# Kernel optimization log

Hardware: AMD Instinct MI355X
Metric: run time of the kernel (lower is better)

The kernel has to match this reference:

```python
import jax, jax.numpy as jnp
import numpy as np

N = 100000  # nodes
E = 800000  # edges (before self-loops)
D = 64      # in_dim == out_dim


def setup_inputs() -> dict:
    key = jax.random.key(0)
    k_x, k_e, k_w, k_b = jax.random.split(key, 4)
    x = jax.random.normal(k_x, (N, D), dtype=jnp.float32)
    edge_index = jax.random.randint(k_e, (2, E), 0, N, dtype=jnp.int64)
    # GCNConv linear params (PyG: glorot weight, zero bias; random here)
    W = jax.random.normal(k_w, (D, D), dtype=jnp.float32) / np.sqrt(D)
    b = jax.random.normal(k_b, (D,), dtype=jnp.float32) * 0.01
    return {"x": x, "W": W, "b": b, "edge_index": edge_index}


def reference(x, W, b, edge_index):
    n = x.shape[0]
    # GCNConv: linear transform first
    h = x @ W.T  # [N, D]
    # add self-loops (PyG default add_self_loops=True)
    loops = jnp.arange(n, dtype=edge_index.dtype)
    src = jnp.concatenate([edge_index[0], loops])
    dst = jnp.concatenate([edge_index[1], loops])
    # symmetric normalization D^{-1/2} A D^{-1/2} (degrees include self-loops)
    deg = jax.ops.segment_sum(jnp.ones_like(dst, dtype=h.dtype), dst, num_segments=n)
    dinv = jnp.where(deg > 0, jax.lax.rsqrt(deg), 0.0)
    norm = dinv[src] * dinv[dst]  # [E+N]
    # gather -> scale -> scatter-add
    msg = h[src] * norm[:, None]  # [E+N, D]
    agg = jax.ops.segment_sum(msg, dst, num_segments=n) + b  # [N, D]
    # residual (in_dim == out_dim -> identity residual) + ReLU
    return jax.nn.relu(agg + x)
```

## Files before the change

### kernel.cpp

```cpp
#include <hip/hip_runtime.h>


#define NN 100000
#define NE 800000
#define DD 64
#define CAP 32
#define CHUNK 1024
#define NCHUNK ((NE + CHUNK - 1) / CHUNK)

typedef unsigned int uint;
typedef unsigned short ushort;

__device__ __forceinline__ ushort f2bf(float f) {
    uint u = __float_as_uint(f);
    u += 0x7fffu + ((u >> 16) & 1u);
    return (ushort)(u >> 16);
}
__device__ __forceinline__ float bflo(uint u) { return __uint_as_float(u << 16); }
__device__ __forceinline__ float bfhi(uint u) { return __uint_as_float(u & 0xffff0000u); }

__global__ __launch_bounds__(256) void fill_kernel(const int* __restrict__ ei,
                                                   int* __restrict__ cur,
                                                   int* __restrict__ srcIdx) {
    int g = blockIdx.x & 7;
    int chunk = blockIdx.x >> 3;
    int base = chunk * CHUNK + threadIdx.x * 4;
    if (base >= NE) return;
    int4 dv = *(const int4*)(ei + NE + base);
    int dd[4] = {dv.x, dv.y, dv.z, dv.w};
#pragma unroll
    for (int j = 0; j < 4; ++j) {
        int d = dd[j];
        if ((d & 7) == g) {
            int s = ei[base + j];
            int c = atomicAdd(&cur[d], 1);
            if (c < CAP) srcIdx[(d << 5) + c] = s;
        }
    }
}

__global__ __launch_bounds__(256) void linear_kernel(const float4* __restrict__ x4g,
                                                     const float* __restrict__ W,
                                                     const int* __restrict__ deg,
                                                     ushort4* __restrict__ hq4) {
    __shared__ float4 wt4[64 * 16];
    __shared__ float4 xs4[64 * 17];
    int t = threadIdx.x;

    float* wt = (float*)wt4;
    for (int m = t; m < 4096; m += 256)
        wt[m] = W[(m & 63) * 64 + (m >> 6)];

    int rowBase = blockIdx.x * 64;
    for (int m = t; m < 1024; m += 256) {
        int rl = m >> 4;
        xs4[rl * 17 + (m & 15)] = (rowBase + rl < NN)
            ? x4g[(size_t)rowBase * 16 + m]
            : make_float4(0.f, 0.f, 0.f, 0.f);
    }
    __syncthreads();

    int tc = t & 15;
    int tr = t >> 4;
    float4 acc[4];
#pragma unroll
    for (int i = 0; i < 4; ++i) acc[i] = make_float4(0.f, 0.f, 0.f, 0.f);

#pragma unroll 2
    for (int kq = 0; kq < 16; ++kq) {
        float4 w0 = wt4[(kq * 4 + 0) * 16 + tc];
        float4 w1 = wt4[(kq * 4 + 1) * 16 + tc];
        float4 w2 = wt4[(kq * 4 + 2) * 16 + tc];
        float4 w3 = wt4[(kq * 4 + 3) * 16 + tc];
#pragma unroll
        for (int i = 0; i < 4; ++i) {
            float4 xv = xs4[(tr * 4 + i) * 17 + kq];
            acc[i].x += xv.x * w0.x + xv.y * w1.x + xv.z * w2.x + xv.w * w3.x;
            acc[i].y += xv.x * w0.y + xv.y * w1.y + xv.z * w2.y + xv.w * w3.y;
            acc[i].z += xv.x * w0.z + xv.y * w1.z + xv.z * w2.z + xv.w * w3.z;
            acc[i].w += xv.x * w0.w + xv.y * w1.w + xv.z * w2.w + xv.w * w3.w;
        }
    }

#pragma unroll
    for (int i = 0; i < 4; ++i) {
        int g = rowBase + tr * 4 + i;
        if (g < NN) {
            float sc = rsqrtf((float)deg[g] + 1.0f);
            ushort4 o;
            o.x = f2bf(acc[i].x * sc); o.y = f2bf(acc[i].y * sc);
            o.z = f2bf(acc[i].z * sc); o.w = f2bf(acc[i].w * sc);
            hq4[(size_t)g * 16 + tc] = o;
        }
    }
}

__global__ __launch_bounds__(256) void gather_kernel(const int* __restrict__ srcIdx,
                                                     const int* __restrict__ deg,
                                                     const uint4* __restrict__ hq4,
                                                     const float4* __restrict__ x4,
                                                     const float* __restrict__ b,
                                                     float4* __restrict__ out4) {
    int t = blockIdx.x * blockDim.x + threadIdx.x;
    int node = t >> 3;
    int l = t & 7;
    if (node >= NN) return;

    int dg = deg[node];
    float di = rsqrtf((float)dg + 1.0f);
    if (dg > CAP) dg = CAP;
    int beg = node << 5;
    int end = beg + dg;

    float acc[8];
    uint4 v = hq4[(size_t)node * 8 + l];
    acc[0] = bflo(v.x); acc[1] = bfhi(v.x);
    acc[2] = bflo(v.y); acc[3] = bfhi(v.y);
    acc[4] = bflo(v.z); acc[5] = bfhi(v.z);
    acc[6] = bflo(v.w); acc[7] = bfhi(v.w);

    int p = beg;
    for (; p + 4 <= end; p += 4) {
        int s0 = srcIdx[p];
        int s1 = srcIdx[p + 1];
        int s2 = srcIdx[p + 2];
        int s3 = srcIdx[p + 3];
        uint4 v0 = hq4[(size_t)s0 * 8 + l];
        uint4 v1 = hq4[(size_t)s1 * 8 + l];
        uint4 v2 = hq4[(size_t)s2 * 8 + l];
        uint4 v3 = hq4[(size_t)s3 * 8 + l];
        acc[0] += bflo(v0.x); acc[1] += bfhi(v0.x);
        acc[2] += bflo(v0.y); acc[3] += bfhi(v0.y);
        acc[4] += bflo(v0.z); acc[5] += bfhi(v0.z);
        acc[6] += bflo(v0.w); acc[7] += bfhi(v0.w);
        acc[0] += bflo(v1.x); acc[1] += bfhi(v1.x);
        acc[2] += bflo(v1.y); acc[3] += bfhi(v1.y);
        acc[4] += bflo(v1.z); acc[5] += bfhi(v1.z);
        acc[6] += bflo(v1.w); acc[7] += bfhi(v1.w);
        acc[0] += bflo(v2.x); acc[1] += bfhi(v2.x);
        acc[2] += bflo(v2.y); acc[3] += bfhi(v2.y);
        acc[4] += bflo(v2.z); acc[5] += bfhi(v2.z);
        acc[6] += bflo(v2.w); acc[7] += bfhi(v2.w);
        acc[0] += bflo(v3.x); acc[1] += bfhi(v3.x);
        acc[2] += bflo(v3.y); acc[3] += bfhi(v3.y);
        acc[4] += bflo(v3.z); acc[5] += bfhi(v3.z);
        acc[6] += bflo(v3.w); acc[7] += bfhi(v3.w);
    }
    for (; p < end; ++p) {
        int s0 = srcIdx[p];
        uint4 v0 = hq4[(size_t)s0 * 8 + l];
        acc[0] += bflo(v0.x); acc[1] += bfhi(v0.x);
        acc[2] += bflo(v0.y); acc[3] += bfhi(v0.y);
        acc[4] += bflo(v0.z); acc[5] += bfhi(v0.z);
        acc[6] += bflo(v0.w); acc[7] += bfhi(v0.w);
    }

    float4 xa = x4[(size_t)node * 16 + l * 2];
    float4 xb = x4[(size_t)node * 16 + l * 2 + 1];
    float4 oa, ob;
    int cb = l * 8;
    oa.x = fmaxf(di * acc[0] + b[cb + 0] + xa.x, 0.f);
    oa.y = fmaxf(di * acc[1] + b[cb + 1] + xa.y, 0.f);
    oa.z = fmaxf(di * acc[2] + b[cb + 2] + xa.z, 0.f);
    oa.w = fmaxf(di * acc[3] + b[cb + 3] + xa.w, 0.f);
    ob.x = fmaxf(di * acc[4] + b[cb + 4] + xb.x, 0.f);
    ob.y = fmaxf(di * acc[5] + b[cb + 5] + xb.y, 0.f);
    ob.z = fmaxf(di * acc[6] + b[cb + 6] + xb.z, 0.f);
    ob.w = fmaxf(di * acc[7] + b[cb + 7] + xb.w, 0.f);
    out4[(size_t)node * 16 + l * 2]     = oa;
    out4[(size_t)node * 16 + l * 2 + 1] = ob;
}

extern "C" void kernel_launch(void* const* d_in, const int* in_sizes, int n_in,
                              void* d_out, int out_size, void* d_ws, size_t ws_size,
                              hipStream_t stream) {
    const float* x = (const float*)d_in[0];
    const float* W = (const float*)d_in[1];
    const float* b = (const float*)d_in[2];
    const int* ei = (const int*)d_in[3];

    char* ws = (char*)d_ws;
    int*    cur    = (int*)(ws + 0);
    int*    srcIdx = (int*)(ws + 400000);
    ushort* hq     = (ushort*)(ws + 13200000);

    hipMemsetAsync(cur, 0, NN * sizeof(int), stream);

    fill_kernel<<<NCHUNK * 8, 256, 0, stream>>>(ei, cur, srcIdx);
    linear_kernel<<<(NN + 63) / 64, 256, 0, stream>>>((const float4*)x, W, cur,
                                                      (ushort4*)hq);
    gather_kernel<<<NN / 32, 256, 0, stream>>>(srcIdx, cur, (const uint4*)hq,
                                               (const float4*)x, b, (float4*)d_out);
}
```

Before: 167.0 us.

## Fuse zero, fill, linear and dinv phases into one cooperative persistent kernel

Replaces the memset, fill kernel and linear kernel with a single cooperative-launch persistent kernel that zeroes degree counters, builds the bucketed adjacency, runs the linear transform and computes dinv, separated by grid-wide syncs. The linear output is no longer pre-scaled by the source degree, so it no longer has to wait for the degree counts. This lets the linear transform overlap with the atomic fill. The gather kernel now loads a per-source dinv value and multiplies it into every accumulated message, adding one extra random load and more multiplies per edge. The goal is to remove launch overhead and inter-kernel serialization, at the cost of grid syncs and a heavier inner gather loop.

```diff
diff --git a/kernel.cpp b/kernel.cpp
--- a/kernel.cpp
+++ b/kernel.cpp
@@ -1,12 +1,16 @@
 #include <hip/hip_runtime.h>
+#include <hip/hip_cooperative_groups.h>
+
+namespace cg = cooperative_groups;
 
 
 #define NN 100000
 #define NE 800000
-#define DD 64
 #define CAP 32
 #define CHUNK 1024
 #define NCHUNK ((NE + CHUNK - 1) / CHUNK)
+#define NUNIT (NCHUNK * 8)
+#define NTILE ((NN + 63) / 64)
 
 typedef unsigned int uint;
 typedef unsigned short ushort;
@@ -19,30 +23,38 @@
 __device__ __forceinline__ float bflo(uint u) { return __uint_as_float(u << 16); }
 __device__ __forceinline__ float bfhi(uint u) { return __uint_as_float(u & 0xffff0000u); }
 
-__global__ __launch_bounds__(256) void fill_kernel(const int* __restrict__ ei,
-                                                   int* __restrict__ cur,
-                                                   int* __restrict__ srcIdx) {
-    int g = blockIdx.x & 7;
-    int chunk = blockIdx.x >> 3;
-    int base = chunk * CHUNK + threadIdx.x * 4;
-    if (base >= NE) return;
-    int4 dv = *(const int4*)(ei + NE + base);
-    int dd[4] = {dv.x, dv.y, dv.z, dv.w};
-#pragma unroll
-    for (int j = 0; j < 4; ++j) {
-        int d = dd[j];
-        if ((d & 7) == g) {
-            int s = ei[base + j];
-            int c = atomicAdd(&cur[d], 1);
-            if (c < CAP) srcIdx[(d << 5) + c] = s;
-        }
-    }
-}
-
-__global__ __launch_bounds__(256) void linear_kernel(const float4* __restrict__ x4g,
-                                                     const float* __restrict__ W,
-                                                     const int* __restrict__ deg,
-                                                     ushort4* __restrict__ hq4) {
+
+__device__ __forceinline__ void zero_phase(int* __restrict__ cur, int bid, int grid) {
+    for (int i = bid * 256 + (int)threadIdx.x; i < NN; i += grid * 256) cur[i] = 0;
+}
+
+__device__ __forceinline__ void fill_phase(const int* __restrict__ ei,
+                                           int* __restrict__ cur,
+                                           int* __restrict__ srcIdx,
+                                           int bid, int grid) {
+    int g = bid & 7;
+    for (int u = bid; u < NUNIT; u += grid) {
+        int base = (u >> 3) * CHUNK + (int)threadIdx.x * 4;
+        if (base < NE) {
+            int4 dv = *(const int4*)(ei + NE + base);
+            int dd[4] = {dv.x, dv.y, dv.z, dv.w};
+#pragma unroll
+            for (int j = 0; j < 4; ++j) {
+                int d = dd[j];
+                if ((d & 7) == g) {
+                    int s = ei[base + j];
+                    int c = atomicAdd(&cur[d], 1);
+                    if (c < CAP) srcIdx[(d << 5) + c] = s;
+                }
+            }
+        }
+    }
+}
+
+__device__ __forceinline__ void linear_phase(const float4* __restrict__ x4g,
+                                             const float* __restrict__ W,
+                                             ushort4* __restrict__ hq4,
+                                             int bid, int grid) {
     __shared__ float4 wt4[64 * 16];
     __shared__ float4 xs4[64 * 17];
     int t = threadIdx.x;
@@ -51,52 +63,93 @@
     for (int m = t; m < 4096; m += 256)
         wt[m] = W[(m & 63) * 64 + (m >> 6)];
 
-    int rowBase = blockIdx.x * 64;
-    for (int m = t; m < 1024; m += 256) {
-        int rl = m >> 4;
-        xs4[rl * 17 + (m & 15)] = (rowBase + rl < NN)
-            ? x4g[(size_t)rowBase * 16 + m]
-            : make_float4(0.f, 0.f, 0.f, 0.f);
-    }
-    __syncthreads();
-
-    int tc = t & 15;
-    int tr = t >> 4;
-    float4 acc[4];
-#pragma unroll
-    for (int i = 0; i < 4; ++i) acc[i] = make_float4(0.f, 0.f, 0.f, 0.f);
+    for (int tile = bid; tile < NTILE; tile += grid) {
+        __syncthreads();
+        int rowBase = tile * 64;
+        for (int m = t; m < 1024; m += 256) {
+            int rl = m >> 4;
+            xs4[rl * 17 + (m & 15)] = (rowBase + rl < NN)
+                ? x4g[(size_t)rowBase * 16 + m]
+                : make_float4(0.f, 0.f, 0.f, 0.f);
+        }
+        __syncthreads();
+
+        int tc = t & 15;
+        int tr = t >> 4;
+        float4 acc[4];
+#pragma unroll
+        for (int i = 0; i < 4; ++i) acc[i] = make_float4(0.f, 0.f, 0.f, 0.f);
 
 #pragma unroll 2
-    for (int kq = 0; kq < 16; ++kq) {
-        float4 w0 = wt4[(kq * 4 + 0) * 16 + tc];
-        float4 w1 = wt4[(kq * 4 + 1) * 16 + tc];
-        float4 w2 = wt4[(kq * 4 + 2) * 16 + tc];
-        float4 w3 = wt4[(kq * 4 + 3) * 16 + tc];
+        for (int kq = 0; kq < 16; ++kq) {
+            float4 w0 = wt4[(kq * 4 + 0) * 16 + tc];
+            float4 w1 = wt4[(kq * 4 + 1) * 16 + tc];
+            float4 w2 = wt4[(kq * 4 + 2) * 16 + tc];
+            float4 w3 = wt4[(kq * 4 + 3) * 16 + tc];
+#pragma unroll
+            for (int i = 0; i < 4; ++i) {
+                float4 xv = xs4[(tr * 4 + i) * 17 + kq];
+                acc[i].x += xv.x * w0.x + xv.y * w1.x + xv.z * w2.x + xv.w * w3.x;
+                acc[i].y += xv.x * w0.y + xv.y * w1.y + xv.z * w2.y + xv.w * w3.y;
+                acc[i].z += xv.x * w0.z + xv.y * w1.z + xv.z * w2.z + xv.w * w3.z;
+                acc[i].w += xv.x * w0.w + xv.y * w1.w + xv.z * w2.w + xv.w * w3.w;
+            }
+        }
+
 #pragma unroll
         for (int i = 0; i < 4; ++i) {
-            float4 xv = xs4[(tr * 4 + i) * 17 + kq];
-            acc[i].x += xv.x * w0.x + xv.y * w1.x + xv.z * w2.x + xv.w * w3.x;
-            acc[i].y += xv.x * w0.y + xv.y * w1.y + xv.z * w2.y + xv.w * w3.y;
-            acc[i].z += xv.x * w0.z + xv.y * w1.z + xv.z * w2.z + xv.w * w3.z;
-            acc[i].w += xv.x * w0.w + xv.y * w1.w + xv.z * w2.w + xv.w * w3.w;
-        }
-    }
-
-#pragma unroll
-    for (int i = 0; i < 4; ++i) {
-        int g = rowBase + tr * 4 + i;
-        if (g < NN) {
-            float sc = rsqrtf((float)deg[g] + 1.0f);
-            ushort4 o;
-            o.x = f2bf(acc[i].x * sc); o.y = f2bf(acc[i].y * sc);
-            o.z = f2bf(acc[i].z * sc); o.w = f2bf(acc[i].w * sc);
-            hq4[(size_t)g * 16 + tc] = o;
-        }
-    }
+            int gr = rowBase + tr * 4 + i;
+            if (gr < NN) {
+                ushort4 o;
+                o.x = f2bf(acc[i].x); o.y = f2bf(acc[i].y);
+                o.z = f2bf(acc[i].z); o.w = f2bf(acc[i].w);
+                hq4[(size_t)gr * 16 + tc] = o;
+            }
+        }
+    }
+}
+
+__device__ __forceinline__ void dinv_phase(const int* __restrict__ cur,
+                                           float* __restrict__ dinv,
+                                           int bid, int grid) {
+    for (int i = bid * 256 + (int)threadIdx.x; i < NN; i += grid * 256)
+        dinv[i] = rsqrtf((float)cur[i] + 1.0f);
+}
+
+__global__ __launch_bounds__(256, 4) void fused_kernel(const int* __restrict__ ei,
+                                                       const float4* __restrict__ x4g,
+                                                       const float* __restrict__ W,
+                                                       int* __restrict__ cur,
+                                                       int* __restrict__ srcIdx,
+                                                       ushort4* __restrict__ hq4,
+                                                       float* __restrict__ dinv) {
+    cg::grid_group gg = cg::this_grid();
+    int bid = blockIdx.x, grid = gridDim.x;
+    zero_phase(cur, bid, grid);
+    gg.sync();
+    fill_phase(ei, cur, srcIdx, bid, grid);
+    linear_phase(x4g, W, hq4, bid, grid);
+    gg.sync();
+    dinv_phase(cur, dinv, bid, grid);
+}
+
+__global__ __launch_bounds__(256) void zero_kernel(int* cur) {
+    zero_phase(cur, blockIdx.x, gridDim.x);
+}
+__global__ __launch_bounds__(256) void fill_kernel(const int* ei, int* cur, int* srcIdx) {
+    fill_phase(ei, cur, srcIdx, blockIdx.x, gridDim.x);
+}
+__global__ __launch_bounds__(256) void linear_kernel(const float4* x4g, const float* W,
+                                                     ushort4* hq4) {
+    linear_phase(x4g, W, hq4, blockIdx.x, gridDim.x);
+}
+__global__ __launch_bounds__(256) void dinv_kernel(const int* cur, float* dinv) {
+    dinv_phase(cur, dinv, blockIdx.x, gridDim.x);
 }
 
 __global__ __launch_bounds__(256) void gather_kernel(const int* __restrict__ srcIdx,
                                                      const int* __restrict__ deg,
+                                                     const float* __restrict__ dinv,
                                                      const uint4* __restrict__ hq4,
                                                      const float4* __restrict__ x4,
                                                      const float* __restrict__ b,
@@ -107,17 +160,17 @@
     if (node >= NN) return;
 
     int dg = deg[node];
-    float di = rsqrtf((float)dg + 1.0f);
+    float di = dinv[node];
     if (dg > CAP) dg = CAP;
     int beg = node << 5;
     int end = beg + dg;
 
     float acc[8];
     uint4 v = hq4[(size_t)node * 8 + l];
-    acc[0] = bflo(v.x); acc[1] = bfhi(v.x);
-    acc[2] = bflo(v.y); acc[3] = bfhi(v.y);
-    acc[4] = bflo(v.z); acc[5] = bfhi(v.z);
-    acc[6] = bflo(v.w); acc[7] = bfhi(v.w);
+    acc[0] = di * bflo(v.x); acc[1] = di * bfhi(v.x);
+    acc[2] = di * bflo(v.y); acc[3] = di * bfhi(v.y);
+    acc[4] = di * bflo(v.z); acc[5] = di * bfhi(v.z);
+    acc[6] = di * bflo(v.w); acc[7] = di * bfhi(v.w);
 
     int p = beg;
     for (; p + 4 <= end; p += 4) {
@@ -125,34 +178,36 @@
         int s1 = srcIdx[p + 1];
         int s2 = srcIdx[p + 2];
         int s3 = srcIdx[p + 3];
+        float w0 = dinv[s0], w1 = dinv[s1], w2 = dinv[s2], w3 = dinv[s3];
         uint4 v0 = hq4[(size_t)s0 * 8 + l];
         uint4 v1 = hq4[(size_t)s1 * 8 + l];
         uint4 v2 = hq4[(size_t)s2 * 8 + l];
         uint4 v3 = hq4[(size_t)s3 * 8 + l];
-        acc[0] += bflo(v0.x); acc[1] += bfhi(v0.x);
-        acc[2] += bflo(v0.y); acc[3] += bfhi(v0.y);
-        acc[4] += bflo(v0.z); acc[5] += bfhi(v0.z);
-        acc[6] += bflo(v0.w); acc[7] += bfhi(v0.w);
-        acc[0] += bflo(v1.x); acc[1] += bfhi(v1.x);
-        acc[2] += bflo(v1.y); acc[3] += bfhi(v1.y);
-        acc[4] += bflo(v1.z); acc[5] += bfhi(v1.z);
-        acc[6] += bflo(v1.w); acc[7] += bfhi(v1.w);
-        acc[0] += bflo(v2.x); acc[1] += bfhi(v2.x);
-        acc[2] += bflo(v2.y); acc[3] += bfhi(v2.y);
-        acc[4] += bflo(v2.z); acc[5] += bfhi(v2.z);
-        acc[6] += bflo(v2.w); acc[7] += bfhi(v2.w);
-        acc[0] += bflo(v3.x); acc[1] += bfhi(v3.x);
-        acc[2] += bflo(v3.y); acc[3] += bfhi(v3.y);
-        acc[4] += bflo(v3.z); acc[5] += bfhi(v3.z);
-        acc[6] += bflo(v3.w); acc[7] += bfhi(v3.w);
+        acc[0] += w0 * bflo(v0.x); acc[1] += w0 * bfhi(v0.x);
+        acc[2] += w0 * bflo(v0.y); acc[3] += w0 * bfhi(v0.y);
+        acc[4] += w0 * bflo(v0.z); acc[5] += w0 * bfhi(v0.z);
+        acc[6] += w0 * bflo(v0.w); acc[7] += w0 * bfhi(v0.w);
+        acc[0] += w1 * bflo(v1.x); acc[1] += w1 * bfhi(v1.x);
+        acc[2] += w1 * bflo(v1.y); acc[3] += w1 * bfhi(v1.y);
+        acc[4] += w1 * bflo(v1.z); acc[5] += w1 * bfhi(v1.z);
+        acc[6] += w1 * bflo(v1.w); acc[7] += w1 * bfhi(v1.w);
+        acc[0] += w2 * bflo(v2.x); acc[1] += w2 * bfhi(v2.x);
+        acc[2] += w2 * bflo(v2.y); acc[3] += w2 * bfhi(v2.y);
+        acc[4] += w2 * bflo(v2.z); acc[5] += w2 * bfhi(v2.z);
+        acc[6] += w2 * bflo(v2.w); acc[7] += w2 * bfhi(v2.w);
+        acc[0] += w3 * bflo(v3.x); acc[1] += w3 * bfhi(v3.x);
+        acc[2] += w3 * bflo(v3.y); acc[3] += w3 * bfhi(v3.y);
+        acc[4] += w3 * bflo(v3.z); acc[5] += w3 * bfhi(v3.z);
+        acc[6] += w3 * bflo(v3.w); acc[7] += w3 * bfhi(v3.w);
     }
     for (; p < end; ++p) {
         int s0 = srcIdx[p];
+        float w0 = dinv[s0];
         uint4 v0 = hq4[(size_t)s0 * 8 + l];
-        acc[0] += bflo(v0.x); acc[1] += bfhi(v0.x);
-        acc[2] += bflo(v0.y); acc[3] += bfhi(v0.y);
-        acc[4] += bflo(v0.z); acc[5] += bfhi(v0.z);
-        acc[6] += bflo(v0.w); acc[7] += bfhi(v0.w);
+        acc[0] += w0 * bflo(v0.x); acc[1] += w0 * bfhi(v0.x);
+        acc[2] += w0 * bflo(v0.y); acc[3] += w0 * bfhi(v0.y);
+        acc[4] += w0 * bflo(v0.z); acc[5] += w0 * bfhi(v0.z);
+        acc[6] += w0 * bflo(v0.w); acc[7] += w0 * bfhi(v0.w);
     }
 
     float4 xa = x4[(size_t)node * 16 + l * 2];
@@ -180,15 +235,31 @@
     const int* ei = (const int*)d_in[3];
 
     char* ws = (char*)d_ws;
-    int*    cur    = (int*)(ws + 0);
-    int*    srcIdx = (int*)(ws + 400000);
-    ushort* hq     = (ushort*)(ws + 13200000);
-
-    hipMemsetAsync(cur, 0, NN * sizeof(int), stream);
-
-    fill_kernel<<<NCHUNK * 8, 256, 0, stream>>>(ei, cur, srcIdx);
-    linear_kernel<<<(NN + 63) / 64, 256, 0, stream>>>((const float4*)x, W, cur,
-                                                      (ushort4*)hq);
-    gather_kernel<<<NN / 32, 256, 0, stream>>>(srcIdx, cur, (const uint4*)hq,
-                                               (const float4*)x, b, (float4*)d_out);
-}
+    int*     cur    = (int*)(ws + 0);
+    float*   dinv   = (float*)(ws + 400000);
+    int*     srcIdx = (int*)(ws + 800000);
+    ushort4* hq4    = (ushort4*)(ws + 13600000);
+
+    const float4* x4 = (const float4*)x;
+
+    int maxB = 0;
+    hipOccupancyMaxActiveBlocksPerMultiprocessor(&maxB, fused_kernel, 256, 0);
+    if (maxB < 1) maxB = 1;
+    int gridA = maxB * 256;
+    if (gridA > 2048) gridA = 2048;
+
+    void* args[] = {(void*)&ei, (void*)&x4, (void*)&W, (void*)&cur,
+                    (void*)&srcIdx, (void*)&hq4, (void*)&dinv};
+    hipError_t err = hipLaunchCooperativeKernel((const void*)fused_kernel,
+                                                dim3(gridA), dim3(256), args, 0, stream);
+    if (err != hipSuccess) {
+        zero_kernel<<<(NN + 255) / 256, 256, 0, stream>>>(cur);
+        fill_kernel<<<NUNIT, 256, 0, stream>>>(ei, cur, srcIdx);
+        linear_kernel<<<NTILE, 256, 0, stream>>>(x4, W, hq4);
+        dinv_kernel<<<(NN + 255) / 256, 256, 0, stream>>>(cur, dinv);
+    }
+
+    gather_kernel<<<(NN * 8 + 255) / 256, 256, 0, stream>>>(srcIdx, cur, dinv,
+                                                            (const uint4*)hq4, x4, b,
+                                                            (float4*)d_out);
+}
```

Measured after the change: 279.1 us. +67.2%, slower.

## Fuse edge fill and linear transform into one launch, apply source norm in gather

Applied to the files above, without the earlier changes.

Merges the CSR fill kernel and the linear transform into a single launch whose blocks are split by block index, so the two independent stages can run concurrently. This requires dropping the source-degree scaling from the linear stage; the gather instead loads deg[src] per edge and applies rsqrt weights, with the unroll widened to 8. The linear stage now reads x straight from global memory instead of staging it in shared memory. The gather does more per-edge work and the linear stage does more uncoalesced loads, in exchange for removing one launch and the dependency between the two stages.

```diff
diff --git a/kernel.cpp b/kernel.cpp
--- a/kernel.cpp
+++ b/kernel.cpp
@@ -3,10 +3,11 @@
 
 #define NN 100000
 #define NE 800000
-#define DD 64
 #define CAP 32
 #define CHUNK 1024
 #define NCHUNK ((NE + CHUNK - 1) / CHUNK)
+#define NUNIT (NCHUNK * 8)
+#define NTILE ((NN + 63) / 64)
 
 typedef unsigned int uint;
 typedef unsigned short ushort;
@@ -19,49 +20,45 @@
 __device__ __forceinline__ float bflo(uint u) { return __uint_as_float(u << 16); }
 __device__ __forceinline__ float bfhi(uint u) { return __uint_as_float(u & 0xffff0000u); }
 
-__global__ __launch_bounds__(256) void fill_kernel(const int* __restrict__ ei,
+__global__ __launch_bounds__(256) void prep_kernel(const int* __restrict__ ei,
+                                                   const float4* __restrict__ x4g,
+                                                   const float* __restrict__ W,
                                                    int* __restrict__ cur,
-                                                   int* __restrict__ srcIdx) {
-    int g = blockIdx.x & 7;
-    int chunk = blockIdx.x >> 3;
-    int base = chunk * CHUNK + threadIdx.x * 4;
-    if (base >= NE) return;
-    int4 dv = *(const int4*)(ei + NE + base);
-    int dd[4] = {dv.x, dv.y, dv.z, dv.w};
+                                                   int* __restrict__ srcIdx,
+                                                   ushort4* __restrict__ hq4) {
+    __shared__ float4 wt4[64 * 16];
+    int t = threadIdx.x;
+    int bid = blockIdx.x;
+
+    if (bid < NUNIT) {
+        int g = bid & 7;
+        int base = (bid >> 3) * CHUNK + t * 4;
+        if (base >= NE) return;
+        int4 dv = *(const int4*)(ei + NE + base);
+        int dd[4] = {dv.x, dv.y, dv.z, dv.w};
 #pragma unroll
-    for (int j = 0; j < 4; ++j) {
-        int d = dd[j];
-        if ((d & 7) == g) {
-            int s = ei[base + j];
-            int c = atomicAdd(&cur[d], 1);
-            if (c < CAP) srcIdx[(d << 5) + c] = s;
+        for (int j = 0; j < 4; ++j) {
+            int d = dd[j];
+            if ((d & 7) == g) {
+                int s = ei[base + j];
+                int c = atomicAdd(&cur[d], 1);
+                if (c < CAP) srcIdx[(d << 5) + c] = s;
+            }
         }
+        return;
     }
-}
 
-__global__ __launch_bounds__(256) void linear_kernel(const float4* __restrict__ x4g,
-                                                     const float* __restrict__ W,
-                                                     const int* __restrict__ deg,
-                                                     ushort4* __restrict__ hq4) {
-    __shared__ float4 wt4[64 * 16];
-    __shared__ float4 xs4[64 * 17];
-    int t = threadIdx.x;
+    int tile = bid - NUNIT;
+    int rowBase = tile * 64;
 
     float* wt = (float*)wt4;
     for (int m = t; m < 4096; m += 256)
         wt[m] = W[(m & 63) * 64 + (m >> 6)];
-
-    int rowBase = blockIdx.x * 64;
-    for (int m = t; m < 1024; m += 256) {
-        int rl = m >> 4;
-        xs4[rl * 17 + (m & 15)] = (rowBase + rl < NN)
-            ? x4g[(size_t)rowBase * 16 + m]
-            : make_float4(0.f, 0.f, 0.f, 0.f);
-    }
     __syncthreads();
 
     int tc = t & 15;
     int tr = t >> 4;
+    int r0 = rowBase + tr * 4;
     float4 acc[4];
 #pragma unroll
     for (int i = 0; i < 4; ++i) acc[i] = make_float4(0.f, 0.f, 0.f, 0.f);
@@ -74,7 +71,9 @@
         float4 w3 = wt4[(kq * 4 + 3) * 16 + tc];
 #pragma unroll
         for (int i = 0; i < 4; ++i) {
-            float4 xv = xs4[(tr * 4 + i) * 17 + kq];
+            int r = r0 + i;
+            float4 xv = (r < NN) ? x4g[(size_t)r * 16 + kq]
+                                 : make_float4(0.f, 0.f, 0.f, 0.f);
             acc[i].x += xv.x * w0.x + xv.y * w1.x + xv.z * w2.x + xv.w * w3.x;
             acc[i].y += xv.x * w0.y + xv.y * w1.y + xv.z * w2.y + xv.w * w3.y;
             acc[i].z += xv.x * w0.z + xv.y * w1.z + xv.z * w2.z + xv.w * w3.z;
@@ -84,13 +83,12 @@
 
 #pragma unroll
     for (int i = 0; i < 4; ++i) {
-        int g = rowBase + tr * 4 + i;
-        if (g < NN) {
-            float sc = rsqrtf((float)deg[g] + 1.0f);
+        int gr = r0 + i;
+        if (gr < NN) {
             ushort4 o;
-            o.x = f2bf(acc[i].x * sc); o.y = f2bf(acc[i].y * sc);
-            o.z = f2bf(acc[i].z * sc); o.w = f2bf(acc[i].w * sc);
-            hq4[(size_t)g * 16 + tc] = o;
+            o.x = f2bf(acc[i].x); o.y = f2bf(acc[i].y);
+            o.z = f2bf(acc[i].z); o.w = f2bf(acc[i].w);
+            hq4[(size_t)gr * 16 + tc] = o;
         }
     }
 }
@@ -114,46 +112,52 @@
 
     float acc[8];
     uint4 v = hq4[(size_t)node * 8 + l];
-    acc[0] = bflo(v.x); acc[1] = bfhi(v.x);
-    acc[2] = bflo(v.y); acc[3] = bfhi(v.y);
-    acc[4] = bflo(v.z); acc[5] = bfhi(v.z);
-    acc[6] = bflo(v.w); acc[7] = bfhi(v.w);
+    acc[0] = di * bflo(v.x); acc[1] = di * bfhi(v.x);
+    acc[2] = di * bflo(v.y); acc[3] = di * bfhi(v.y);
+    acc[4] = di * bflo(v.z); acc[5] = di * bfhi(v.z);
+    acc[6] = di * bflo(v.w); acc[7] = di * bfhi(v.w);
 
     int p = beg;
-    for (; p + 4 <= end; p += 4) {
-        int s0 = srcIdx[p];
-        int s1 = srcIdx[p + 1];
-        int s2 = srcIdx[p + 2];
-        int s3 = srcIdx[p + 3];
+#define EDGE_W(sj) rsqrtf((float)deg[sj] + 1.0f)
+#define ACCUM(vj, wj)                                           \
+    acc[0] += wj * bflo(vj.x); acc[1] += wj * bfhi(vj.x);       \
+    acc[2] += wj * bflo(vj.y); acc[3] += wj * bfhi(vj.y);       \
+    acc[4] += wj * bflo(vj.z); acc[5] += wj * bfhi(vj.z);       \
+    acc[6] += wj * bflo(vj.w); acc[7] += wj * bfhi(vj.w)
+
+    for (; p + 8 <= end; p += 8) {
+        int s0 = srcIdx[p],     s1 = srcIdx[p + 1];
+        int s2 = srcIdx[p + 2], s3 = srcIdx[p + 3];
+        int s4 = srcIdx[p + 4], s5 = srcIdx[p + 5];
+        int s6 = srcIdx[p + 6], s7 = srcIdx[p + 7];
         uint4 v0 = hq4[(size_t)s0 * 8 + l];
         uint4 v1 = hq4[(size_t)s1 * 8 + l];
         uint4 v2 = hq4[(size_t)s2 * 8 + l];
         uint4 v3 = hq4[(size_t)s3 * 8 + l];
-        acc[0] += bflo(v0.x); acc[1] += bfhi(v0.x);
-        acc[2] += bflo(v0.y); acc[3] += bfhi(v0.y);
-        acc[4] += bflo(v0.z); acc[5] += bfhi(v0.z);
-        acc[6] += bflo(v0.w); acc[7] += bfhi(v0.w);
-        acc[0] += bflo(v1.x); acc[1] += bfhi(v1.x);
-        acc[2] += bflo(v1.y); acc[3] += bfhi(v1.y);
-        acc[4] += bflo(v1.z); acc[5] += bfhi(v1.z);
-        acc[6] += bflo(v1.w); acc[7] += bfhi(v1.w);
-        acc[0] += bflo(v2.x); acc[1] += bfhi(v2.x);
-        acc[2] += bflo(v2.y); acc[3] += bfhi(v2.y);
-        acc[4] += bflo(v2.z); acc[5] += bfhi(v2.z);
-        acc[6] += bflo(v2.w); acc[7] += bfhi(v2.w);
-        acc[0] += bflo(v3.x); acc[1] += bfhi(v3.x);
-        acc[2] += bflo(v3.y); acc[3] += bfhi(v3.y);
-        acc[4] += bflo(v3.z); acc[5] += bfhi(v3.z);
-        acc[6] += bflo(v3.w); acc[7] += bfhi(v3.w);
+        uint4 v4 = hq4[(size_t)s4 * 8 + l];
+        uint4 v5 = hq4[(size_t)s5 * 8 + l];
+        uint4 v6 = hq4[(size_t)s6 * 8 + l];
+        uint4 v7 = hq4[(size_t)s7 * 8 + l];
+        float w0 = EDGE_W(s0), w1 = EDGE_W(s1), w2 = EDGE_W(s2), w3 = EDGE_W(s3);
+        float w4 = EDGE_W(s4), w5 = EDGE_W(s5), w6 = EDGE_W(s6), w7 = EDGE_W(s7);
+        ACCUM(v0, w0); ACCUM(v1, w1); ACCUM(v2, w2); ACCUM(v3, w3);
+        ACCUM(v4, w4); ACCUM(v5, w5); ACCUM(v6, w6); ACCUM(v7, w7);
     }
-    for (; p < end; ++p) {
+    for (; p + 2 <= end; p += 2) {
+        int s0 = srcIdx[p], s1 = srcIdx[p + 1];
+        uint4 v0 = hq4[(size_t)s0 * 8 + l];
+        uint4 v1 = hq4[(size_t)s1 * 8 + l];
+        float w0 = EDGE_W(s0), w1 = EDGE_W(s1);
+        ACCUM(v0, w0); ACCUM(v1, w1);
+    }
+    if (p < end) {
         int s0 = srcIdx[p];
         uint4 v0 = hq4[(size_t)s0 * 8 + l];
-        acc[0] += bflo(v0.x); acc[1] += bfhi(v0.x);
-        acc[2] += bflo(v0.y); acc[3] += bfhi(v0.y);
-        acc[4] += bflo(v0.z); acc[5] += bfhi(v0.z);
-        acc[6] += bflo(v0.w); acc[7] += bfhi(v0.w);
+        float w0 = EDGE_W(s0);
+        ACCUM(v0, w0);
     }
+#undef ACCUM
+#undef EDGE_W
 
     float4 xa = x4[(size_t)node * 16 + l * 2];
     float4 xb = x4[(size_t)node * 16 + l * 2 + 1];
@@ -180,15 +184,15 @@
     const int* ei = (const int*)d_in[3];
 
     char* ws = (char*)d_ws;
-    int*    cur    = (int*)(ws + 0);
-    int*    srcIdx = (int*)(ws + 400000);
-    ushort* hq     = (ushort*)(ws + 13200000);
+    int*     cur    = (int*)(ws + 0);
+    int*     srcIdx = (int*)(ws + 400000);
+    ushort4* hq4    = (ushort4*)(ws + 13200000);
+
+    const float4* x4 = (const float4*)x;
 
     hipMemsetAsync(cur, 0, NN * sizeof(int), stream);
-
-    fill_kernel<<<NCHUNK * 8, 256, 0, stream>>>(ei, cur, srcIdx);
-    linear_kernel<<<(NN + 63) / 64, 256, 0, stream>>>((const float4*)x, W, cur,
-                                                      (ushort4*)hq);
-    gather_kernel<<<NN / 32, 256, 0, stream>>>(srcIdx, cur, (const uint4*)hq,
-                                               (const float4*)x, b, (float4*)d_out);
+    prep_kernel<<<NUNIT + NTILE, 256, 0, stream>>>(ei, x4, W, cur, srcIdx, hq4);
+    gather_kernel<<<(NN * 8 + 255) / 256, 256, 0, stream>>>(srcIdx, cur,
+                                                            (const uint4*)hq4, x4, b,
+                                                            (float4*)d_out);
 }
```

Result: slower. 180.9 us (+8.3%).
